# Kernel tuning notes

Hardware: AMD Instinct MI355X
Metric: run time of the kernel (lower is better)

## Reference

```python
import jax, jax.numpy as jnp
import numpy as np

D_MODEL = 256
POOL = 10  # Keras MaxPooling1D(pool_size=10) -> stride 10, padding 'same'


def setup_inputs() -> dict:
    key = jax.random.key(0)
    ks = jax.random.split(key, 11)
    B, S, D = 4, 4096, D_MODEL
    scale = 1.0 / np.sqrt(D)
    inp = {
        "v": jax.random.normal(ks[0], (B, S, D), jnp.float32),
        "k": jax.random.normal(ks[1], (B, S, D), jnp.float32),
        "q": jax.random.normal(ks[2], (B, S, D), jnp.float32),
        "wq": jax.random.normal(ks[3], (D, D), jnp.float32) * scale,
        "bq": jnp.zeros((D,), jnp.float32),
        "wk": jax.random.normal(ks[4], (D, D), jnp.float32) * scale,
        "bk": jnp.zeros((D,), jnp.float32),
        "wv": jax.random.normal(ks[5], (D, D), jnp.float32) * scale,
        "bv": jnp.zeros((D,), jnp.float32),
        "wo": jax.random.normal(ks[6], (D, D), jnp.float32) * scale,
        "bo": jnp.zeros((D,), jnp.float32),
    }
    return inp


def reference(v, k, q, wq, bq, wk, bk, wv, bv, wo, bo):
    d = q.shape[-1]
    qp = q @ wq + bq          # [B,Sq,D]
    kp = k @ wk + bk          # [B,Sk,D]
    vp = v @ wv + bv          # [B,Sk,D]
    scores = jnp.einsum('bqd,bkd->bqk', qp, kp) / jnp.sqrt(jnp.float32(d))
    # MaxPooling1D over the steps (Sq) axis, stride = pool_size, 'same' padding
    pooled = jax.lax.reduce_window(
        scores, -jnp.inf, jax.lax.max,
        window_dimensions=(1, POOL, 1),
        window_strides=(1, POOL, 1),
        padding='SAME')          # [B, ceil(Sq/10), Sk]
    attn = jax.nn.softmax(pooled, axis=-1)
    out = jnp.einsum('bqk,bkd->bqd', attn, vp)
    return out @ wo + bo
```

## Files before the change

kernel.cpp:

```cpp
#include <hip/hip_runtime.h>
#include <hip/hip_bf16.h>
#include <stdint.h>

typedef __attribute__((ext_vector_type(8))) short          bf16x8;
typedef __attribute__((ext_vector_type(4))) float          f32x4;
typedef __attribute__((ext_vector_type(4))) float          f4;
typedef __attribute__((ext_vector_type(8))) unsigned short u16x8;
typedef __attribute__((ext_vector_type(4))) unsigned short u16x4;

#define DEVINL __device__ __forceinline__

static constexpr int B  = 4;
static constexpr int S  = 4096;
static constexpr int D  = 256;
static constexpr int SP = 410;

DEVINL unsigned short f2bf(float x) {
  union { float f; unsigned u; } v; v.f = x;
  unsigned r = v.u + 0x7FFFu + ((v.u >> 16) & 1u);
  return (unsigned short)(r >> 16);
}

DEVINL f32x4 mfma16(bf16x8 a, bf16x8 b, f32x4 c) {
  return __builtin_amdgcn_mfma_f32_16x16x32_bf16(a, b, c, 0, 0, 0);
}

typedef const __attribute__((address_space(1))) void* gas_t;
typedef __attribute__((address_space(3))) void*       las_t;
DEVINL void gload16(const void* g, void* l) {
  __builtin_amdgcn_global_load_lds((gas_t)g, (las_t)l, 16, 0, 0);
}

__global__ __launch_bounds__(256) void wt_trans_kernel(
    const float* __restrict__ wq, const float* __restrict__ wk,
    const float* __restrict__ wv, const float* __restrict__ wo,
    unsigned short* __restrict__ wt)
{
  int idx = blockIdx.x * 256 + threadIdx.x;
  int mat = idx >> 16;
  int r   = idx & 65535;
  int n   = r >> 8;
  int k   = r & 255;
  const float* w = (mat == 0) ? wq : (mat == 1) ? wk : (mat == 2) ? wv : wo;
  wt[idx] = f2bf(w[k * 256 + n]);
}

__global__ __launch_bounds__(256) void proj_kernel(
    const float* __restrict__ xq, const float* __restrict__ xk, const float* __restrict__ xv,
    const unsigned short* __restrict__ wt,
    const float* __restrict__ bq, const float* __restrict__ bk, const float* __restrict__ bv,
    unsigned short* __restrict__ qp, unsigned short* __restrict__ kp, unsigned short* __restrict__ vp)
{
  int z = blockIdx.z;
  const float* A            = (z == 0) ? xq : (z == 1) ? xk : xv;
  const unsigned short* W   = wt + z * 65536;
  const float* bias         = (z == 0) ? bq : (z == 1) ? bk : bv;
  unsigned short* Out       = (z == 0) ? qp : (z == 1) ? kp : vp;

  int m0 = blockIdx.x * 128;
  int n0 = blockIdx.y * 128;

  __shared__ unsigned short As[128][40];
  __shared__ unsigned short Bs[128][40];

  int tid  = threadIdx.x;
  int lane = tid & 63, wid = tid >> 6;
  int wr = wid >> 1, wc = wid & 1;
  int lrow = lane & 15, kseg = lane >> 4;

  f32x4 zero4 = {0.f, 0.f, 0.f, 0.f};
  f32x4 acc[4][4];
#pragma unroll
  for (int i = 0; i < 4; i++)
#pragma unroll
    for (int j = 0; j < 4; j++) acc[i][j] = zero4;

  for (int ks = 0; ks < 256; ks += 32) {
    for (int s = tid; s < 1024; s += 256) {
      int row = s >> 3, seg = s & 7;
      f4 v = *reinterpret_cast<const f4*>(&A[(size_t)(m0 + row) * 256 + ks + seg * 4]);
      u16x4 h;
      h[0] = f2bf(v[0]); h[1] = f2bf(v[1]); h[2] = f2bf(v[2]); h[3] = f2bf(v[3]);
      *reinterpret_cast<u16x4*>(&As[row][seg * 4]) = h;
    }
    for (int s = tid; s < 512; s += 256) {
      int row = s >> 2, seg = s & 3;
      u16x8 v = *reinterpret_cast<const u16x8*>(&W[(size_t)(n0 + row) * 256 + ks + seg * 8]);
      *reinterpret_cast<u16x8*>(&Bs[row][seg * 8]) = v;
    }
    __syncthreads();
    bf16x8 af[4], bfr[4];
#pragma unroll
    for (int rf = 0; rf < 4; rf++)
      af[rf] = *reinterpret_cast<const bf16x8*>(&As[wr * 64 + rf * 16 + lrow][kseg * 8]);
#pragma unroll
    for (int cf = 0; cf < 4; cf++)
      bfr[cf] = *reinterpret_cast<const bf16x8*>(&Bs[wc * 64 + cf * 16 + lrow][kseg * 8]);
#pragma unroll
    for (int rf = 0; rf < 4; rf++)
#pragma unroll
      for (int cf = 0; cf < 4; cf++)
        acc[rf][cf] = mfma16(af[rf], bfr[cf], acc[rf][cf]);
    __syncthreads();
  }

  int r4 = (lane >> 4) * 4;
#pragma unroll
  for (int rf = 0; rf < 4; rf++)
#pragma unroll
    for (int cf = 0; cf < 4; cf++) {
      int n = n0 + wc * 64 + cf * 16 + lrow;
      float bv_ = bias[n];
#pragma unroll
      for (int r = 0; r < 4; r++) {
        int m = m0 + wr * 64 + rf * 16 + r4 + r;
        Out[(size_t)m * 256 + n] = f2bf(acc[rf][cf][r] + bv_);
      }
    }
}

__global__ __launch_bounds__(512, 4) void scores_pool_kernel(
    const unsigned short* __restrict__ qp, const unsigned short* __restrict__ kp,
    float* __restrict__ pooled)
{
  int b  = blockIdx.z;
  int wb = blockIdx.y;
  int nb = blockIdx.x;
  int w0 = wb * 25;
  int qb = w0 * 10 - 2;
  int n0 = nb * 128;
  int nwin = SP - w0; if (nwin > 25) nwin = 25;

  __shared__ __align__(16) union SM {
    struct { char A[32768]; char Bm[16384]; } st;
    float pm[9216];
  } sm;
  char* Asm = sm.st.A;
  char* Bsm = sm.st.Bm;

  const unsigned short* qpb = qp + (size_t)b * S * 256;
  const unsigned short* kpb = kp + (size_t)b * S * 256;

  int tid  = threadIdx.x;
  int lane = tid & 63, wid = tid >> 6;
  int wr = wid >> 1, wc = wid & 1;
  int lrow = lane & 15, kseg = lane >> 4;

  f32x4 zero4 = {0.f, 0.f, 0.f, 0.f};
  f32x4 acc[4][4];
#pragma unroll
  for (int i = 0; i < 4; i++)
#pragma unroll
    for (int j = 0; j < 4; j++) acc[i][j] = zero4;

  for (int ks = 0; ks < 4; ++ks) {
#pragma unroll
    for (int i = 0; i < 4; ++i) {
      int inst = wid * 4 + i;
      int sg   = inst * 64 + lane;
      int row  = sg >> 3;
      int c16  = sg & 7;
      int q = qb + row; q = (q < 0) ? 0 : ((q > S - 1) ? (S - 1) : q);
      const char* g = (const char*)qpb + ((size_t)q << 9) + (ks << 7) + ((c16 ^ (row & 7)) << 4);
      gload16(g, Asm + inst * 1024);
    }
#pragma unroll
    for (int i = 0; i < 2; ++i) {
      int inst = wid * 2 + i;
      int sg   = inst * 64 + lane;
      int row  = sg >> 3;
      int c16  = sg & 7;
      const char* g = (const char*)kpb + ((size_t)(n0 + row) << 9) + (ks << 7) + ((c16 ^ (row & 7)) << 4);
      gload16(g, Bsm + inst * 1024);
    }
    __syncthreads();
#pragma unroll
    for (int kk = 0; kk < 2; ++kk) {
      bf16x8 af[4], bfr[4];
#pragma unroll
      for (int mi = 0; mi < 4; ++mi) {
        int R   = wr * 64 + mi * 16 + lrow;
        int c16 = (kk * 4 + kseg) ^ (R & 7);
        af[mi] = *reinterpret_cast<const bf16x8*>(Asm + R * 128 + c16 * 16);
      }
#pragma unroll
      for (int cf = 0; cf < 4; ++cf) {
        int nl  = wc * 64 + cf * 16 + lrow;
        int c16 = (kk * 4 + kseg) ^ (nl & 7);
        bfr[cf] = *reinterpret_cast<const bf16x8*>(Bsm + nl * 128 + c16 * 16);
      }
#pragma unroll
      for (int mi = 0; mi < 4; ++mi)
#pragma unroll
        for (int cf = 0; cf < 4; ++cf)
          acc[mi][cf] = mfma16(af[mi], bfr[cf], acc[mi][cf]);
    }
    __syncthreads();
  }

  int h = kseg;
#pragma unroll
  for (int c = 0; c < 2; ++c) {
    __syncthreads();
    if (wc == c) {
#pragma unroll
      for (int mi = 0; mi < 4; ++mi) {
        int p = wr * 32 + mi * 8 + h * 2;
#pragma unroll
        for (int cf = 0; cf < 4; ++cf) {
          int col = cf * 16 + lrow;
          sm.pm[p * 72 + col]       = fmaxf(acc[mi][cf][0], acc[mi][cf][1]);
          sm.pm[(p + 1) * 72 + col] = fmaxf(acc[mi][cf][2], acc[mi][cf][3]);
        }
      }
    }
    __syncthreads();
    for (int s = tid; s < 1600; s += 512) {
      int j = s >> 6, col = s & 63;
      if (j < nwin) {
        float m = -3.4e38f;
#pragma unroll
        for (int i = 0; i < 5; ++i) {
          int p  = 5 * j + i;
          int q0 = qb + 2 * p;
          if (q0 >= 0 && q0 < S) m = fmaxf(m, sm.pm[p * 72 + col]);
        }
        pooled[((size_t)b * SP + w0 + j) * 4096 + n0 + c * 64 + col] = m * 0.0625f;
      }
    }
  }
}

__global__ __launch_bounds__(256) void softmax_kernel(
    const float* __restrict__ pooled, unsigned short* __restrict__ attn)
{
  int row = blockIdx.x;
  const float* p = pooled + (size_t)row * 4096;
  unsigned short* a = attn + (size_t)row * 4096;
  int tid = threadIdx.x;
  int lane = tid & 63, wid = tid >> 6;

  f4 v[4];
  float mx = -3.4e38f;
#pragma unroll
  for (int i = 0; i < 4; i++) {
    v[i] = *reinterpret_cast<const f4*>(&p[i * 1024 + tid * 4]);
    mx = fmaxf(mx, fmaxf(fmaxf(v[i][0], v[i][1]), fmaxf(v[i][2], v[i][3])));
  }
#pragma unroll
  for (int off = 32; off > 0; off >>= 1) mx = fmaxf(mx, __shfl_xor(mx, off, 64));
  __shared__ float redm[4];
  __shared__ float reds[4];
  if (lane == 0) redm[wid] = mx;
  __syncthreads();
  mx = fmaxf(fmaxf(redm[0], redm[1]), fmaxf(redm[2], redm[3]));

  float e[16];
  float sum = 0.f;
#pragma unroll
  for (int i = 0; i < 4; i++)
#pragma unroll
    for (int j = 0; j < 4; j++) {
      float t = __expf(v[i][j] - mx);
      e[i * 4 + j] = t;
      sum += t;
    }
#pragma unroll
  for (int off = 32; off > 0; off >>= 1) sum += __shfl_xor(sum, off, 64);
  if (lane == 0) reds[wid] = sum;
  __syncthreads();
  sum = reds[0] + reds[1] + reds[2] + reds[3];
  float inv = 1.f / sum;
#pragma unroll
  for (int i = 0; i < 4; i++) {
    u16x4 o;
#pragma unroll
    for (int j = 0; j < 4; j++) o[j] = f2bf(e[i * 4 + j] * inv);
    *reinterpret_cast<u16x4*>(&a[i * 1024 + tid * 4]) = o;
  }
}

__global__ __launch_bounds__(256) void vpt_kernel(
    const unsigned short* __restrict__ vp, unsigned short* __restrict__ vpT)
{
  int b  = blockIdx.y;
  int kt = blockIdx.x >> 2;
  int dt = blockIdx.x & 3;
  int k0 = kt * 64, d0 = dt * 64;

  __shared__ unsigned short t[64][66];
  const unsigned short* src = vp + (size_t)b * S * 256;
  unsigned short* dst = vpT + (size_t)b * 256 * S;

  int tid = threadIdx.x;
  for (int s = tid; s < 512; s += 256) {
    int r = s >> 3, seg = s & 7;
    u16x8 v = *reinterpret_cast<const u16x8*>(&src[(size_t)(k0 + r) * 256 + d0 + seg * 8]);
#pragma unroll
    for (int j = 0; j < 4; j++) {
      unsigned short* pp = &t[r][seg * 8 + j * 2];
      pp[0] = v[j * 2]; pp[1] = v[j * 2 + 1];
    }
  }
  __syncthreads();
  int d  = tid >> 2;
  int kb = (tid & 3) * 16;
  u16x8 o0, o1;
#pragma unroll
  for (int j = 0; j < 8; j++) o0[j] = t[kb + j][d];
#pragma unroll
  for (int j = 0; j < 8; j++) o1[j] = t[kb + 8 + j][d];
  *reinterpret_cast<u16x8*>(&dst[(size_t)(d0 + d) * S + k0 + kb])     = o0;
  *reinterpret_cast<u16x8*>(&dst[(size_t)(d0 + d) * S + k0 + kb + 8]) = o1;
}

__global__ __launch_bounds__(256) void pv_kernel(
    const unsigned short* __restrict__ attn, const unsigned short* __restrict__ vpT,
    float* __restrict__ part)
{
  int bx = blockIdx.x;
  int b  = bx >> 2, mt = bx & 3;
  int m0 = mt * 128;
  int n0 = blockIdx.y * 128;
  int kz = blockIdx.z;
  int k0 = kz * 512;

  const unsigned short* Ab = attn + (size_t)b * SP * 4096;
  const unsigned short* Bb = vpT  + (size_t)b * 256 * 4096;
  float* Pz = part + (size_t)kz * 419840;

  __shared__ unsigned short As[128][40];
  __shared__ unsigned short Bs[128][40];

  int tid  = threadIdx.x;
  int lane = tid & 63, wid = tid >> 6;
  int wr = wid >> 1, wc = wid & 1;
  int lrow = lane & 15, kseg = lane >> 4;

  f32x4 zero4 = {0.f, 0.f, 0.f, 0.f};
  f32x4 acc[4][4];
#pragma unroll
  for (int i = 0; i < 4; i++)
#pragma unroll
    for (int j = 0; j < 4; j++) acc[i][j] = zero4;

  for (int ks = k0; ks < k0 + 512; ks += 32) {
    for (int s = tid; s < 512; s += 256) {
      int row = s >> 2, seg = s & 3;
      int m = m0 + row; m = (m > SP - 1) ? (SP - 1) : m;
      u16x8 v = *reinterpret_cast<const u16x8*>(&Ab[(size_t)m * 4096 + ks + seg * 8]);
      *reinterpret_cast<u16x8*>(&As[row][seg * 8]) = v;
    }
    for (int s = tid; s < 512; s += 256) {
      int row = s >> 2, seg = s & 3;
      u16x8 v = *reinterpret_cast<const u16x8*>(&Bb[(size_t)(n0 + row) * 4096 + ks + seg * 8]);
      *reinterpret_cast<u16x8*>(&Bs[row][seg * 8]) = v;
    }
    __syncthreads();
    bf16x8 af[4], bfr[4];
#pragma unroll
    for (int rf = 0; rf < 4; rf++)
      af[rf] = *reinterpret_cast<const bf16x8*>(&As[wr * 64 + rf * 16 + lrow][kseg * 8]);
#pragma unroll
    for (int cf = 0; cf < 4; cf++)
      bfr[cf] = *reinterpret_cast<const bf16x8*>(&Bs[wc * 64 + cf * 16 + lrow][kseg * 8]);
#pragma unroll
    for (int rf = 0; rf < 4; rf++)
#pragma unroll
      for (int cf = 0; cf < 4; cf++)
        acc[rf][cf] = mfma16(af[rf], bfr[cf], acc[rf][cf]);
    __syncthreads();
  }

  int r4 = (lane >> 4) * 4;
#pragma unroll
  for (int rf = 0; rf < 4; rf++)
#pragma unroll
    for (int cf = 0; cf < 4; cf++) {
      int n = n0 + wc * 64 + cf * 16 + lrow;
#pragma unroll
      for (int r = 0; r < 4; r++) {
        int m = m0 + wr * 64 + rf * 16 + r4 + r;
        if (m < SP) Pz[((size_t)b * SP + m) * 256 + n] = acc[rf][cf][r];
      }
    }
}

__global__ __launch_bounds__(256) void out_kernel(
    const float* __restrict__ part, const unsigned short* __restrict__ woT,
    const float* __restrict__ bo, float* __restrict__ out)
{
  int m0 = blockIdx.x * 128;
  int n0 = blockIdx.y * 128;
  const int M = B * SP;

  __shared__ unsigned short As[128][40];
  __shared__ unsigned short Bs[128][40];

  int tid  = threadIdx.x;
  int lane = tid & 63, wid = tid >> 6;
  int wr = wid >> 1, wc = wid & 1;
  int lrow = lane & 15, kseg = lane >> 4;

  f32x4 zero4 = {0.f, 0.f, 0.f, 0.f};
  f32x4 acc[4][4];
#pragma unroll
  for (int i = 0; i < 4; i++)
#pragma unroll
    for (int j = 0; j < 4; j++) acc[i][j] = zero4;

  for (int ks = 0; ks < 256; ks += 32) {
    for (int s = tid; s < 1024; s += 256) {
      int row = s >> 3, seg = s & 7;
      int m = m0 + row; m = (m > M - 1) ? (M - 1) : m;
      const float* p0 = part + (size_t)m * 256 + ks + seg * 4;
      f4 a = {0.f, 0.f, 0.f, 0.f};
#pragma unroll
      for (int z = 0; z < 8; ++z) a += *reinterpret_cast<const f4*>(p0 + (size_t)z * 419840);
      u16x4 hh;
      hh[0] = f2bf(a[0]); hh[1] = f2bf(a[1]); hh[2] = f2bf(a[2]); hh[3] = f2bf(a[3]);
      *reinterpret_cast<u16x4*>(&As[row][seg * 4]) = hh;
    }
    for (int s = tid; s < 512; s += 256) {
      int row = s >> 2, seg = s & 3;
      u16x8 v = *reinterpret_cast<const u16x8*>(&woT[(size_t)(n0 + row) * 256 + ks + seg * 8]);
      *reinterpret_cast<u16x8*>(&Bs[row][seg * 8]) = v;
    }
    __syncthreads();
    bf16x8 af[4], bfr[4];
#pragma unroll
    for (int rf = 0; rf < 4; rf++)
      af[rf] = *reinterpret_cast<const bf16x8*>(&As[wr * 64 + rf * 16 + lrow][kseg * 8]);
#pragma unroll
    for (int cf = 0; cf < 4; cf++)
      bfr[cf] = *reinterpret_cast<const bf16x8*>(&Bs[wc * 64 + cf * 16 + lrow][kseg * 8]);
#pragma unroll
    for (int rf = 0; rf < 4; rf++)
#pragma unroll
      for (int cf = 0; cf < 4; cf++)
        acc[rf][cf] = mfma16(af[rf], bfr[cf], acc[rf][cf]);
    __syncthreads();
  }

  int r4 = (lane >> 4) * 4;
#pragma unroll
  for (int rf = 0; rf < 4; rf++)
#pragma unroll
    for (int cf = 0; cf < 4; cf++) {
      int n = n0 + wc * 64 + cf * 16 + lrow;
      float bv_ = bo[n];
#pragma unroll
      for (int r = 0; r < 4; r++) {
        int m = m0 + wr * 64 + rf * 16 + r4 + r;
        if (m < M) out[(size_t)m * 256 + n] = acc[rf][cf][r] + bv_;
      }
    }
}

extern "C" void kernel_launch(void* const* d_in, const int* in_sizes, int n_in,
                              void* d_out, int out_size, void* d_ws, size_t ws_size,
                              hipStream_t stream)
{
  const float* v  = (const float*)d_in[0];
  const float* k  = (const float*)d_in[1];
  const float* q  = (const float*)d_in[2];
  const float* wq = (const float*)d_in[3];
  const float* bq = (const float*)d_in[4];
  const float* wk = (const float*)d_in[5];
  const float* bk = (const float*)d_in[6];
  const float* wv = (const float*)d_in[7];
  const float* bv = (const float*)d_in[8];
  const float* wo = (const float*)d_in[9];
  const float* bo = (const float*)d_in[10];
  float* out = (float*)d_out;

  char* ws = (char*)d_ws;
  size_t off = 0;
  auto alloc = [&](size_t bytes) -> void* {
    void* p = ws + off;
    off += (bytes + 255) & ~(size_t)255;
    return p;
  };
  unsigned short* qp   = (unsigned short*)alloc((size_t)B * S * D * 2);
  unsigned short* kp   = (unsigned short*)alloc((size_t)B * S * D * 2);
  unsigned short* vp   = (unsigned short*)alloc((size_t)B * S * D * 2);
  unsigned short* vpT  = (unsigned short*)alloc((size_t)B * S * D * 2);
  unsigned short* wt   = (unsigned short*)alloc((size_t)4 * 256 * 256 * 2);
  float*          pooled = (float*)alloc((size_t)B * SP * 4096 * 4);
  unsigned short* attn = (unsigned short*)alloc((size_t)B * SP * 4096 * 2);
  float*          part = pooled;

  wt_trans_kernel<<<1024, 256, 0, stream>>>(wq, wk, wv, wo, wt);
  proj_kernel<<<dim3(128, 2, 3), 256, 0, stream>>>(q, k, v, wt, bq, bk, bv, qp, kp, vp);
  scores_pool_kernel<<<dim3(32, 17, 4), 512, 0, stream>>>(qp, kp, pooled);
  softmax_kernel<<<B * SP, 256, 0, stream>>>(pooled, attn);
  vpt_kernel<<<dim3(256, 4), 256, 0, stream>>>(vp, vpT);
  pv_kernel<<<dim3(16, 2, 8), 256, 0, stream>>>(attn, vpT, part);
  out_kernel<<<dim3(13, 2), 256, 0, stream>>>(part, wt + 3 * 65536, bo, out);
}
```

Baseline: 257.5 us.

## Double-buffer GEMM kernels with async LDS loads and split bf16 conversion and reduction

Moves the fp32-to-bf16 input conversion out of the projection GEMM into its own kernel. All GEMM kernels (proj, scores, pv, out) now stage tiles through double-buffered swizzled LDS using global_load_lds, so the next tile loads while the current one is multiplied. The PV split-K factor goes from 8 to 16, with a separate reduce kernel that writes a bf16 context for the output GEMM. Proj and out now use 256-row tiles with 512 threads. This adds kernel launches and extra global traffic for the converted inputs and partial sums, and the doubled LDS footprint may lower occupancy.

```diff
diff --git a/kernel.cpp b/kernel.cpp
--- a/kernel.cpp
+++ b/kernel.cpp
@@ -14,6 +14,9 @@
 static constexpr int S  = 4096;
 static constexpr int D  = 256;
 static constexpr int SP = 410;
+static constexpr int KZ = 16;
+static constexpr int MO = B * SP;
+static constexpr size_t PSLICE = (size_t)MO * D;
 
 DEVINL unsigned short f2bf(float x) {
   union { float f; unsigned u; } v; v.f = x;
@@ -45,23 +48,41 @@
   wt[idx] = f2bf(w[k * 256 + n]);
 }
 
-__global__ __launch_bounds__(256) void proj_kernel(
+__global__ __launch_bounds__(256) void cvt_kernel(
     const float* __restrict__ xq, const float* __restrict__ xk, const float* __restrict__ xv,
-    const unsigned short* __restrict__ wt,
+    unsigned short* __restrict__ oq, unsigned short* __restrict__ ok, unsigned short* __restrict__ ov)
+{
+  int z = blockIdx.y;
+  const float* x    = (z == 0) ? xq : (z == 1) ? xk : xv;
+  unsigned short* o = (z == 0) ? oq : (z == 1) ? ok : ov;
+  size_t i = ((size_t)blockIdx.x * 256 + threadIdx.x) * 8;
+  f4 a = *reinterpret_cast<const f4*>(x + i);
+  f4 c = *reinterpret_cast<const f4*>(x + i + 4);
+  u16x8 h;
+  h[0] = f2bf(a[0]); h[1] = f2bf(a[1]); h[2] = f2bf(a[2]); h[3] = f2bf(a[3]);
+  h[4] = f2bf(c[0]); h[5] = f2bf(c[1]); h[6] = f2bf(c[2]); h[7] = f2bf(c[3]);
+  *reinterpret_cast<u16x8*>(o + i) = h;
+}
+
+__global__ __launch_bounds__(512) void proj_kernel(
+    const unsigned short* __restrict__ xq, const unsigned short* __restrict__ xk,
+    const unsigned short* __restrict__ xv, const unsigned short* __restrict__ wt,
     const float* __restrict__ bq, const float* __restrict__ bk, const float* __restrict__ bv,
     unsigned short* __restrict__ qp, unsigned short* __restrict__ kp, unsigned short* __restrict__ vp)
 {
   int z = blockIdx.z;
-  const float* A            = (z == 0) ? xq : (z == 1) ? xk : xv;
-  const unsigned short* W   = wt + z * 65536;
-  const float* bias         = (z == 0) ? bq : (z == 1) ? bk : bv;
-  unsigned short* Out       = (z == 0) ? qp : (z == 1) ? kp : vp;
-
-  int m0 = blockIdx.x * 128;
+  const unsigned short* X = (z == 0) ? xq : (z == 1) ? xk : xv;
+  const unsigned short* W = wt + z * 65536;
+  const float* bias       = (z == 0) ? bq : (z == 1) ? bk : bv;
+  unsigned short* Out     = (z == 0) ? qp : (z == 1) ? kp : vp;
+
+  int m0 = blockIdx.x * 256;
   int n0 = blockIdx.y * 128;
 
-  __shared__ unsigned short As[128][40];
-  __shared__ unsigned short Bs[128][40];
+  __shared__ __align__(16) struct { char A[2][32768]; char Bm[2][16384]; } sm;
+
+  const char* Xc = (const char*)X;
+  const char* Wc = (const char*)W;
 
   int tid  = threadIdx.x;
   int lane = tid & 63, wid = tid >> 6;
@@ -75,51 +96,73 @@
 #pragma unroll
     for (int j = 0; j < 4; j++) acc[i][j] = zero4;
 
-  for (int ks = 0; ks < 256; ks += 32) {
-    for (int s = tid; s < 1024; s += 256) {
-      int row = s >> 3, seg = s & 7;
-      f4 v = *reinterpret_cast<const f4*>(&A[(size_t)(m0 + row) * 256 + ks + seg * 4]);
-      u16x4 h;
-      h[0] = f2bf(v[0]); h[1] = f2bf(v[1]); h[2] = f2bf(v[2]); h[3] = f2bf(v[3]);
-      *reinterpret_cast<u16x4*>(&As[row][seg * 4]) = h;
-    }
-    for (int s = tid; s < 512; s += 256) {
-      int row = s >> 2, seg = s & 3;
-      u16x8 v = *reinterpret_cast<const u16x8*>(&W[(size_t)(n0 + row) * 256 + ks + seg * 8]);
-      *reinterpret_cast<u16x8*>(&Bs[row][seg * 8]) = v;
+  auto stage = [&](int t, int buf) {
+#pragma unroll
+    for (int i = 0; i < 4; ++i) {
+      int inst = wid * 4 + i;
+      int sg   = inst * 64 + lane;
+      int row  = sg >> 3, c16 = sg & 7;
+      gload16(Xc + ((size_t)(m0 + row) << 9) + (t << 7) + ((c16 ^ (row & 7)) << 4),
+              sm.A[buf] + inst * 1024);
+    }
+#pragma unroll
+    for (int i = 0; i < 2; ++i) {
+      int inst = wid * 2 + i;
+      int sg   = inst * 64 + lane;
+      int row  = sg >> 3, c16 = sg & 7;
+      gload16(Wc + ((size_t)(n0 + row) << 9) + (t << 7) + ((c16 ^ (row & 7)) << 4),
+              sm.Bm[buf] + inst * 1024);
+    }
+  };
+
+  stage(0, 0);
+  __syncthreads();
+#pragma unroll
+  for (int t = 0; t < 4; ++t) {
+    int cur = t & 1;
+    if (t < 3) stage(t + 1, cur ^ 1);
+    const char* Asm = sm.A[cur];
+    const char* Bsm = sm.Bm[cur];
+#pragma unroll
+    for (int kk = 0; kk < 2; ++kk) {
+      bf16x8 af[4], bfr[4];
+#pragma unroll
+      for (int mi = 0; mi < 4; ++mi) {
+        int R = wr * 64 + mi * 16 + lrow;
+        int c16 = (kk * 4 + kseg) ^ (R & 7);
+        af[mi] = *reinterpret_cast<const bf16x8*>(Asm + R * 128 + c16 * 16);
+      }
+#pragma unroll
+      for (int cf = 0; cf < 4; ++cf) {
+        int nl = wc * 64 + cf * 16 + lrow;
+        int c16 = (kk * 4 + kseg) ^ (nl & 7);
+        bfr[cf] = *reinterpret_cast<const bf16x8*>(Bsm + nl * 128 + c16 * 16);
+      }
+#pragma unroll
+      for (int mi = 0; mi < 4; ++mi)
+#pragma unroll
+        for (int cf = 0; cf < 4; ++cf)
+          acc[mi][cf] = mfma16(af[mi], bfr[cf], acc[mi][cf]);
     }
     __syncthreads();
-    bf16x8 af[4], bfr[4];
-#pragma unroll
-    for (int rf = 0; rf < 4; rf++)
-      af[rf] = *reinterpret_cast<const bf16x8*>(&As[wr * 64 + rf * 16 + lrow][kseg * 8]);
-#pragma unroll
-    for (int cf = 0; cf < 4; cf++)
-      bfr[cf] = *reinterpret_cast<const bf16x8*>(&Bs[wc * 64 + cf * 16 + lrow][kseg * 8]);
-#pragma unroll
-    for (int rf = 0; rf < 4; rf++)
-#pragma unroll
-      for (int cf = 0; cf < 4; cf++)
-        acc[rf][cf] = mfma16(af[rf], bfr[cf], acc[rf][cf]);
-    __syncthreads();
-  }
-
-  int r4 = (lane >> 4) * 4;
-#pragma unroll
-  for (int rf = 0; rf < 4; rf++)
+  }
+
+  int r4 = kseg * 4;
+#pragma unroll
+  for (int mi = 0; mi < 4; mi++)
 #pragma unroll
     for (int cf = 0; cf < 4; cf++) {
       int n = n0 + wc * 64 + cf * 16 + lrow;
       float bv_ = bias[n];
 #pragma unroll
       for (int r = 0; r < 4; r++) {
-        int m = m0 + wr * 64 + rf * 16 + r4 + r;
-        Out[(size_t)m * 256 + n] = f2bf(acc[rf][cf][r] + bv_);
-      }
-    }
-}
-
-__global__ __launch_bounds__(512, 4) void scores_pool_kernel(
+        int m = m0 + wr * 64 + mi * 16 + r4 + r;
+        Out[(size_t)m * 256 + n] = f2bf(acc[mi][cf][r] + bv_);
+      }
+    }
+}
+
+__global__ __launch_bounds__(512) void scores_pool_kernel(
     const unsigned short* __restrict__ qp, const unsigned short* __restrict__ kp,
     float* __restrict__ pooled)
 {
@@ -132,14 +175,12 @@
   int nwin = SP - w0; if (nwin > 25) nwin = 25;
 
   __shared__ __align__(16) union SM {
-    struct { char A[32768]; char Bm[16384]; } st;
+    struct { char A[2][32768]; char Bm[2][16384]; } st;
     float pm[9216];
   } sm;
-  char* Asm = sm.st.A;
-  char* Bsm = sm.st.Bm;
-
-  const unsigned short* qpb = qp + (size_t)b * S * 256;
-  const unsigned short* kpb = kp + (size_t)b * S * 256;
+
+  const char* qpc = (const char*)(qp + (size_t)b * S * 256);
+  const char* kpc = (const char*)(kp + (size_t)b * S * 256);
 
   int tid  = threadIdx.x;
   int lane = tid & 63, wid = tid >> 6;
@@ -153,39 +194,46 @@
 #pragma unroll
     for (int j = 0; j < 4; j++) acc[i][j] = zero4;
 
-  for (int ks = 0; ks < 4; ++ks) {
+  auto stage = [&](int t, int buf) {
 #pragma unroll
     for (int i = 0; i < 4; ++i) {
       int inst = wid * 4 + i;
       int sg   = inst * 64 + lane;
-      int row  = sg >> 3;
-      int c16  = sg & 7;
+      int row  = sg >> 3, c16 = sg & 7;
       int q = qb + row; q = (q < 0) ? 0 : ((q > S - 1) ? (S - 1) : q);
-      const char* g = (const char*)qpb + ((size_t)q << 9) + (ks << 7) + ((c16 ^ (row & 7)) << 4);
-      gload16(g, Asm + inst * 1024);
+      gload16(qpc + ((size_t)q << 9) + (t << 7) + ((c16 ^ (row & 7)) << 4),
+              sm.st.A[buf] + inst * 1024);
     }
 #pragma unroll
     for (int i = 0; i < 2; ++i) {
       int inst = wid * 2 + i;
       int sg   = inst * 64 + lane;
-      int row  = sg >> 3;
-      int c16  = sg & 7;
-      const char* g = (const char*)kpb + ((size_t)(n0 + row) << 9) + (ks << 7) + ((c16 ^ (row & 7)) << 4);
-      gload16(g, Bsm + inst * 1024);
-    }
-    __syncthreads();
+      int row  = sg >> 3, c16 = sg & 7;
+      gload16(kpc + ((size_t)(n0 + row) << 9) + (t << 7) + ((c16 ^ (row & 7)) << 4),
+              sm.st.Bm[buf] + inst * 1024);
+    }
+  };
+
+  stage(0, 0);
+  __syncthreads();
+#pragma unroll
+  for (int t = 0; t < 4; ++t) {
+    int cur = t & 1;
+    if (t < 3) stage(t + 1, cur ^ 1);
+    const char* Asm = sm.st.A[cur];
+    const char* Bsm = sm.st.Bm[cur];
 #pragma unroll
     for (int kk = 0; kk < 2; ++kk) {
       bf16x8 af[4], bfr[4];
 #pragma unroll
       for (int mi = 0; mi < 4; ++mi) {
-        int R   = wr * 64 + mi * 16 + lrow;
+        int R = wr * 64 + mi * 16 + lrow;
         int c16 = (kk * 4 + kseg) ^ (R & 7);
         af[mi] = *reinterpret_cast<const bf16x8*>(Asm + R * 128 + c16 * 16);
       }
 #pragma unroll
       for (int cf = 0; cf < 4; ++cf) {
-        int nl  = wc * 64 + cf * 16 + lrow;
+        int nl = wc * 64 + cf * 16 + lrow;
         int c16 = (kk * 4 + kseg) ^ (nl & 7);
         bfr[cf] = *reinterpret_cast<const bf16x8*>(Bsm + nl * 128 + c16 * 16);
       }
@@ -323,14 +371,13 @@
   int m0 = mt * 128;
   int n0 = blockIdx.y * 128;
   int kz = blockIdx.z;
-  int k0 = kz * 512;
-
-  const unsigned short* Ab = attn + (size_t)b * SP * 4096;
-  const unsigned short* Bb = vpT  + (size_t)b * 256 * 4096;
-  float* Pz = part + (size_t)kz * 419840;
-
-  __shared__ unsigned short As[128][40];
-  __shared__ unsigned short Bs[128][40];
+  int k0b = kz * 512;
+
+  const char* Ac = (const char*)(attn + (size_t)b * SP * 4096);
+  const char* Bc = (const char*)(vpT  + (size_t)b * 256 * 4096);
+  float* Pz = part + (size_t)kz * PSLICE;
+
+  __shared__ __align__(16) struct { char A[2][16384]; char Bm[2][16384]; } sm;
 
   int tid  = threadIdx.x;
   int lane = tid & 63, wid = tid >> 6;
@@ -344,58 +391,93 @@
 #pragma unroll
     for (int j = 0; j < 4; j++) acc[i][j] = zero4;
 
-  for (int ks = k0; ks < k0 + 512; ks += 32) {
-    for (int s = tid; s < 512; s += 256) {
-      int row = s >> 2, seg = s & 3;
+  auto stage = [&](int t, int buf) {
+#pragma unroll
+    for (int i = 0; i < 4; ++i) {
+      int inst = wid * 4 + i;
+      int sg   = inst * 64 + lane;
+      int row  = sg >> 3, c16 = sg & 7;
       int m = m0 + row; m = (m > SP - 1) ? (SP - 1) : m;
-      u16x8 v = *reinterpret_cast<const u16x8*>(&Ab[(size_t)m * 4096 + ks + seg * 8]);
-      *reinterpret_cast<u16x8*>(&As[row][seg * 8]) = v;
-    }
-    for (int s = tid; s < 512; s += 256) {
-      int row = s >> 2, seg = s & 3;
-      u16x8 v = *reinterpret_cast<const u16x8*>(&Bb[(size_t)(n0 + row) * 4096 + ks + seg * 8]);
-      *reinterpret_cast<u16x8*>(&Bs[row][seg * 8]) = v;
+      gload16(Ac + (size_t)m * 8192 + k0b + (t << 7) + ((c16 ^ (row & 7)) << 4),
+              sm.A[buf] + inst * 1024);
+    }
+#pragma unroll
+    for (int i = 0; i < 4; ++i) {
+      int inst = wid * 4 + i;
+      int sg   = inst * 64 + lane;
+      int row  = sg >> 3, c16 = sg & 7;
+      gload16(Bc + (size_t)(n0 + row) * 8192 + k0b + (t << 7) + ((c16 ^ (row & 7)) << 4),
+              sm.Bm[buf] + inst * 1024);
+    }
+  };
+
+  stage(0, 0);
+  __syncthreads();
+#pragma unroll
+  for (int t = 0; t < 4; ++t) {
+    int cur = t & 1;
+    if (t < 3) stage(t + 1, cur ^ 1);
+    const char* Asm = sm.A[cur];
+    const char* Bsm = sm.Bm[cur];
+#pragma unroll
+    for (int kk = 0; kk < 2; ++kk) {
+      bf16x8 af[4], bfr[4];
+#pragma unroll
+      for (int mi = 0; mi < 4; ++mi) {
+        int R = wr * 64 + mi * 16 + lrow;
+        int c16 = (kk * 4 + kseg) ^ (R & 7);
+        af[mi] = *reinterpret_cast<const bf16x8*>(Asm + R * 128 + c16 * 16);
+      }
+#pragma unroll
+      for (int cf = 0; cf < 4; ++cf) {
+        int nl = wc * 64 + cf * 16 + lrow;
+        int c16 = (kk * 4 + kseg) ^ (nl & 7);
+        bfr[cf] = *reinterpret_cast<const bf16x8*>(Bsm + nl * 128 + c16 * 16);
+      }
+#pragma unroll
+      for (int mi = 0; mi < 4; ++mi)
+#pragma unroll
+        for (int cf = 0; cf < 4; ++cf)
+          acc[mi][cf] = mfma16(af[mi], bfr[cf], acc[mi][cf]);
     }
     __syncthreads();
-    bf16x8 af[4], bfr[4];
-#pragma unroll
-    for (int rf = 0; rf < 4; rf++)
-      af[rf] = *reinterpret_cast<const bf16x8*>(&As[wr * 64 + rf * 16 + lrow][kseg * 8]);
-#pragma unroll
-    for (int cf = 0; cf < 4; cf++)
-      bfr[cf] = *reinterpret_cast<const bf16x8*>(&Bs[wc * 64 + cf * 16 + lrow][kseg * 8]);
-#pragma unroll
-    for (int rf = 0; rf < 4; rf++)
-#pragma unroll
-      for (int cf = 0; cf < 4; cf++)
-        acc[rf][cf] = mfma16(af[rf], bfr[cf], acc[rf][cf]);
-    __syncthreads();
-  }
-
-  int r4 = (lane >> 4) * 4;
-#pragma unroll
-  for (int rf = 0; rf < 4; rf++)
+  }
+
+  int r4 = kseg * 4;
+#pragma unroll
+  for (int mi = 0; mi < 4; mi++)
 #pragma unroll
     for (int cf = 0; cf < 4; cf++) {
       int n = n0 + wc * 64 + cf * 16 + lrow;
 #pragma unroll
       for (int r = 0; r < 4; r++) {
-        int m = m0 + wr * 64 + rf * 16 + r4 + r;
-        if (m < SP) Pz[((size_t)b * SP + m) * 256 + n] = acc[rf][cf][r];
-      }
-    }
-}
-
-__global__ __launch_bounds__(256) void out_kernel(
-    const float* __restrict__ part, const unsigned short* __restrict__ woT,
+        int m = m0 + wr * 64 + mi * 16 + r4 + r;
+        if (m < SP) Pz[((size_t)b * SP + m) * 256 + n] = acc[mi][cf][r];
+      }
+    }
+}
+
+__global__ __launch_bounds__(256) void reduce_kernel(
+    const float* __restrict__ part, unsigned short* __restrict__ ctxb)
+{
+  size_t i = (size_t)blockIdx.x * 256 + threadIdx.x;
+  float s = 0.f;
+#pragma unroll
+  for (int z = 0; z < KZ; ++z) s += part[z * PSLICE + i];
+  ctxb[i] = f2bf(s);
+}
+
+__global__ __launch_bounds__(512) void out_kernel(
+    const unsigned short* __restrict__ ctxb, const unsigned short* __restrict__ woT,
     const float* __restrict__ bo, float* __restrict__ out)
 {
-  int m0 = blockIdx.x * 128;
+  int m0 = blockIdx.x * 256;
   int n0 = blockIdx.y * 128;
-  const int M = B * SP;
-
-  __shared__ unsigned short As[128][40];
-  __shared__ unsigned short Bs[128][40];
+
+  __shared__ __align__(16) struct { char A[2][32768]; char Bm[2][16384]; } sm;
+
+  const char* Xc = (const char*)ctxb;
+  const char* Wc = (const char*)woT;
 
   int tid  = threadIdx.x;
   int lane = tid & 63, wid = tid >> 6;
@@ -409,50 +491,69 @@
 #pragma unroll
     for (int j = 0; j < 4; j++) acc[i][j] = zero4;
 
-  for (int ks = 0; ks < 256; ks += 32) {
-    for (int s = tid; s < 1024; s += 256) {
-      int row = s >> 3, seg = s & 7;
-      int m = m0 + row; m = (m > M - 1) ? (M - 1) : m;
-      const float* p0 = part + (size_t)m * 256 + ks + seg * 4;
-      f4 a = {0.f, 0.f, 0.f, 0.f};
-#pragma unroll
-      for (int z = 0; z < 8; ++z) a += *reinterpret_cast<const f4*>(p0 + (size_t)z * 419840);
-      u16x4 hh;
-      hh[0] = f2bf(a[0]); hh[1] = f2bf(a[1]); hh[2] = f2bf(a[2]); hh[3] = f2bf(a[3]);
-      *reinterpret_cast<u16x4*>(&As[row][seg * 4]) = hh;
-    }
-    for (int s = tid; s < 512; s += 256) {
-      int row = s >> 2, seg = s & 3;
-      u16x8 v = *reinterpret_cast<const u16x8*>(&woT[(size_t)(n0 + row) * 256 + ks + seg * 8]);
-      *reinterpret_cast<u16x8*>(&Bs[row][seg * 8]) = v;
+  auto stage = [&](int t, int buf) {
+#pragma unroll
+    for (int i = 0; i < 4; ++i) {
+      int inst = wid * 4 + i;
+      int sg   = inst * 64 + lane;
+      int row  = sg >> 3, c16 = sg & 7;
+      int m = m0 + row; m = (m > MO - 1) ? (MO - 1) : m;
+      gload16(Xc + ((size_t)m << 9) + (t << 7) + ((c16 ^ (row & 7)) << 4),
+              sm.A[buf] + inst * 1024);
+    }
+#pragma unroll
+    for (int i = 0; i < 2; ++i) {
+      int inst = wid * 2 + i;
+      int sg   = inst * 64 + lane;
+      int row  = sg >> 3, c16 = sg & 7;
+      gload16(Wc + ((size_t)(n0 + row) << 9) + (t << 7) + ((c16 ^ (row & 7)) << 4),
+              sm.Bm[buf] + inst * 1024);
+    }
+  };
+
+  stage(0, 0);
+  __syncthreads();
+#pragma unroll
+  for (int t = 0; t < 4; ++t) {
+    int cur = t & 1;
+    if (t < 3) stage(t + 1, cur ^ 1);
+    const char* Asm = sm.A[cur];
+    const char* Bsm = sm.Bm[cur];
+#pragma unroll
+    for (int kk = 0; kk < 2; ++kk) {
+      bf16x8 af[4], bfr[4];
+#pragma unroll
+      for (int mi = 0; mi < 4; ++mi) {
+        int R = wr * 64 + mi * 16 + lrow;
+        int c16 = (kk * 4 + kseg) ^ (R & 7);
+        af[mi] = *reinterpret_cast<const bf16x8*>(Asm + R * 128 + c16 * 16);
+      }
+#pragma unroll
+      for (int cf = 0; cf < 4; ++cf) {
+        int nl = wc * 64 + cf * 16 + lrow;
+        int c16 = (kk * 4 + kseg) ^ (nl & 7);
+        bfr[cf] = *reinterpret_cast<const bf16x8*>(Bsm + nl * 128 + c16 * 16);
+      }
+#pragma unroll
+      for (int mi = 0; mi < 4; ++mi)
+#pragma unroll
+        for (int cf = 0; cf < 4; ++cf)
+          acc[mi][cf] = mfma16(af[mi], bfr[cf], acc[mi][cf]);
     }
     __syncthreads();
-    bf16x8 af[4], bfr[4];
-#pragma unroll
-    for (int rf = 0; rf < 4; rf++)
-      af[rf] = *reinterpret_cast<const bf16x8*>(&As[wr * 64 + rf * 16 + lrow][kseg * 8]);
-#pragma unroll
-    for (int cf = 0; cf < 4; cf++)
-      bfr[cf] = *reinterpret_cast<const bf16x8*>(&Bs[wc * 64 + cf * 16 + lrow][kseg * 8]);
-#pragma unroll
-    for (int rf = 0; rf < 4; rf++)
-#pragma unroll
-      for (int cf = 0; cf < 4; cf++)
-        acc[rf][cf] = mfma16(af[rf], bfr[cf], acc[rf][cf]);
-    __syncthreads();
-  }
-
-  int r4 = (lane >> 4) * 4;
-#pragma unroll
-  for (int rf = 0; rf < 4; rf++)
+  }
+
+  int r4 = kseg * 4;
+#pragma unroll
+  for (int mi = 0; mi < 4; mi++)
 #pragma unroll
     for (int cf = 0; cf < 4; cf++) {
       int n = n0 + wc * 64 + cf * 16 + lrow;
       float bv_ = bo[n];
 #pragma unroll
       for (int r = 0; r < 4; r++) {
-        int m = m0 + wr * 64 + rf * 16 + r4 + r;
-        if (m < M) out[(size_t)m * 256 + n] = acc[rf][cf][r] + bv_;
+        int m = m0 + wr * 64 + mi * 16 + r4 + r;
+        if (m < MO) out[(size_t)m * 256 + n] = acc[mi][cf][r] + bv_;
       }
     }
 }
@@ -486,15 +587,23 @@
   unsigned short* vp   = (unsigned short*)alloc((size_t)B * S * D * 2);
   unsigned short* vpT  = (unsigned short*)alloc((size_t)B * S * D * 2);
   unsigned short* wt   = (unsigned short*)alloc((size_t)4 * 256 * 256 * 2);
-  float*          pooled = (float*)alloc((size_t)B * SP * 4096 * 4);
+  unsigned short* ctxb = (unsigned short*)alloc(PSLICE * 2);
+  char* shared_region  = (char*)alloc((size_t)B * SP * 4096 * 4);
   unsigned short* attn = (unsigned short*)alloc((size_t)B * SP * 4096 * 2);
-  float*          part = pooled;
+
+  unsigned short* qx = (unsigned short*)shared_region;
+  unsigned short* kx = qx + (size_t)B * S * D;
+  unsigned short* vx = kx + (size_t)B * S * D;
+  float* pooled = (float*)shared_region;
+  float* part   = (float*)shared_region;
 
   wt_trans_kernel<<<1024, 256, 0, stream>>>(wq, wk, wv, wo, wt);
-  proj_kernel<<<dim3(128, 2, 3), 256, 0, stream>>>(q, k, v, wt, bq, bk, bv, qp, kp, vp);
+  cvt_kernel<<<dim3(2048, 3), 256, 0, stream>>>(q, k, v, qx, kx, vx);
+  proj_kernel<<<dim3(64, 2, 3), 512, 0, stream>>>(qx, kx, vx, wt, bq, bk, bv, qp, kp, vp);
   scores_pool_kernel<<<dim3(32, 17, 4), 512, 0, stream>>>(qp, kp, pooled);
   softmax_kernel<<<B * SP, 256, 0, stream>>>(pooled, attn);
   vpt_kernel<<<dim3(256, 4), 256, 0, stream>>>(vp, vpT);
-  pv_kernel<<<dim3(16, 2, 8), 256, 0, stream>>>(attn, vpT, part);
-  out_kernel<<<dim3(13, 2), 256, 0, stream>>>(part, wt + 3 * 65536, bo, out);
-}
+  pv_kernel<<<dim3(16, 2, KZ), 256, 0, stream>>>(attn, vpT, part);
+  reduce_kernel<<<(int)(PSLICE / 256), 256, 0, stream>>>(part, ctxb);
+  out_kernel<<<dim3(7, 2), 512, 0, stream>>>(ctxb, wt + 3 * 65536, bo, out);
+}
```

New measurement: 230.2 us. -10.6%, faster.
